# Optimization experiments

Hardware: AMD Instinct MI355X
Metric: run time of the kernel (lower is better)

## Reference

```python
import jax, jax.numpy as jnp
import numpy as np

N = 50000          # masked node count
E = 800000         # edges (avg degree 16)
IN_DIM, GCN_DIM, REL_DIM, TRAIN_DIM, OUT_DIM = 3, 128, 64, 128, 2
BATCHES = 1


def setup_inputs() -> dict:
    key = jax.random.key(0)
    ks = jax.random.split(key, 16)
    s = 0.05
    return {
        "features": jax.random.normal(ks[0], (N, IN_DIM), jnp.float32),
        "edge_index": jax.random.randint(ks[1], (2, E), 0, N, dtype=jnp.int32),
        "trainOT": jax.random.normal(ks[2], (TRAIN_DIM,), jnp.float32),
        "W1": jax.random.normal(ks[3], (IN_DIM, GCN_DIM), jnp.float32) * s,
        "b1": jnp.zeros((GCN_DIM,), jnp.float32),
        "W2": jax.random.normal(ks[4], (GCN_DIM, GCN_DIM), jnp.float32) * s,
        "b2": jnp.zeros((GCN_DIM,), jnp.float32),
        "Wq": jax.random.normal(ks[5], (GCN_DIM, REL_DIM), jnp.float32) * s,
        "bq": jnp.zeros((REL_DIM,), jnp.float32),
        "Wk": jax.random.normal(ks[6], (TRAIN_DIM, REL_DIM), jnp.float32) * s,
        "bk": jnp.zeros((REL_DIM,), jnp.float32),
        "Wv": jax.random.normal(ks[7], (GCN_DIM, TRAIN_DIM), jnp.float32) * s,
        "bv": jnp.zeros((TRAIN_DIM,), jnp.float32),
        "Ws": jax.random.normal(ks[8], (TRAIN_DIM, OUT_DIM * N), jnp.float32) * s,
        "bs": jnp.zeros((OUT_DIM * N,), jnp.float32),
    }


def _gcn_conv(x, W, b, src, dst, n):
    """PyG GCNConv: h = D^-1/2 (A+I) D^-1/2 (x W) + b (self-loops already in src/dst)."""
    h = x @ W                                                  # [n, d_out]
    ones = jnp.ones(src.shape[0], dtype=x.dtype)
    deg = jax.ops.segment_sum(ones, dst, num_segments=n)      # in-degree incl. self-loop
    dinv = jnp.where(deg > 0, jax.lax.rsqrt(deg), 0.0)
    norm = dinv[src] * dinv[dst]                               # [E+n]
    msg = h[src] * norm[:, None]                               # gather (dominant traffic)
    return jax.ops.segment_sum(msg, dst, num_segments=n) + b   # scatter-add


def reference(features, edge_index, trainOT, W1, b1, W2, b2, Wq, bq, Wk, bk, Wv, bv, Ws, bs):
    n = features.shape[0]
    loop = jnp.arange(n, dtype=edge_index.dtype)
    src = jnp.concatenate([edge_index[0], loop])
    dst = jnp.concatenate([edge_index[1], loop])

    h1 = jax.nn.relu(_gcn_conv(features, W1, b1, src, dst, n))   # gcn1 + relu
    h2 = _gcn_conv(h1, W2, b2, src, dst, n)                      # gcn2

    q = h2 @ Wq + bq                                             # [n, rel]
    v = h2 @ Wv + bv                                             # [n, train]
    k = trainOT @ Wk + bk                                        # [rel]
    scale = jnp.asarray(Wq.shape[1], q.dtype) ** 0.5
    rel = jax.nn.sigmoid((q @ k) / scale)                        # [n]
    summed_idea = (rel[:, None] * v).sum(axis=0)                 # [train]
    new_trainOT = trainOT + summed_idea
    speak = new_trainOT @ Ws + bs                                # [out_dim * num_nodes]
    out = speak.reshape(BATCHES, -1, OUT_DIM)
    return out, new_trainOT
```

## Files before the change

### kernel.cpp

```cpp
#include <hip/hip_runtime.h>
#include <math.h>

#define O_ROWPTR (256*1024)
#define O_DINV   (512*1024)
#define O_SMALL  (768*1024)
#define O_GHIST  (1024*1024)
#define O_BSTART (1256*1024)
#define O_GOFF   (1280*1024)
#define O_SORT   (1536*1024)
#define O_PART   (1536*1024)
#define O_XS     (4800*1024)
#define O_COL    (5760*1024)
#define O_H1     (9216*1024)

#define LAYER2_BLOCKS 2048
#define NCHUNK 256

static __device__ __forceinline__ unsigned int f2bf(float f) {
    unsigned int u = __float_as_uint(f);
    return (u + 0x7fffu + ((u >> 16) & 1u)) >> 16;
}
static __device__ __forceinline__ float bf_lo(unsigned int w) { return __uint_as_float(w << 16); }
static __device__ __forceinline__ float bf_hi(unsigned int w) { return __uint_as_float(w & 0xffff0000u); }

static __device__ __forceinline__ int blockExclScan256(int v, volatile int* lds, int t) {
    int lane = t & 63, wid = t >> 6;
    int incl = v;
#pragma unroll
    for (int off = 1; off < 64; off <<= 1) {
        int n = __shfl_up(incl, off);
        if (lane >= off) incl += n;
    }
    if (lane == 63) lds[wid] = incl;
    __syncthreads();
    if (t == 0) {
        int s = 0;
#pragma unroll
        for (int i = 0; i < 4; ++i) { int x = lds[i]; lds[i] = s; s += x; }
    }
    __syncthreads();
    return lds[wid] + incl - v;
}

__global__ void k_hist(const int* __restrict__ dst, int* __restrict__ ghist,
                       int E, int CS, int NB) {
    __shared__ int lh[256];
    int b = blockIdx.x, t = threadIdx.x;
    lh[t] = 0; __syncthreads();
    int s = b * CS, e = min(E, s + CS);
    for (int i = s + t; i < e; i += 256) {
        atomicAdd(&lh[dst[i] >> 8], 1);
    }
    __syncthreads();
    if (t < NB) ghist[t * NCHUNK + b] = lh[t];
}

__global__ void k_bstart(const int* __restrict__ ghist, int* __restrict__ bstart, int NB) {
    __shared__ int lds[4];
    int t = threadIdx.x;
    int v = 0;
    if (t < NB) {
        const int* row = ghist + t * NCHUNK;
        for (int b = 0; b < NCHUNK; ++b) v += row[b];
    }
    int ex = blockExclScan256(v, lds, t);
    if (t <= NB) bstart[t] = ex;
}

__global__ void k_goff(const int* __restrict__ ghist, const int* __restrict__ bstart,
                       int* __restrict__ goff, int NB) {
    __shared__ int lds1[4];
    int nb = blockIdx.x, t = threadIdx.x;
    int base = bstart[nb];
    int g = ghist[nb * NCHUNK + t];
    int gx = blockExclScan256(g, lds1, t);
    goff[nb * NCHUNK + t] = base + gx;
}

__global__ void k_scatter(const int* __restrict__ src, const int* __restrict__ dst,
                          const int* __restrict__ goff, unsigned int* __restrict__ sorted,
                          int E, int CS, int NB) {
    __shared__ int lcur[256];
    int b = blockIdx.x, t = threadIdx.x;
    if (t < NB) lcur[t] = goff[t * NCHUNK + b];
    __syncthreads();
    int s = b * CS, e = min(E, s + CS);
    for (int i = s + t; i < e; i += 256) {
        int d = dst[i];
        int pos = atomicAdd(&lcur[d >> 8], 1);
        sorted[pos] = ((unsigned int)(d & 255) << 16) | (unsigned int)src[i];
    }
}

__global__ void k_build(const unsigned int* __restrict__ sorted, const int* __restrict__ bstart,
                        int* __restrict__ row_ptr, int* __restrict__ col,
                        float* __restrict__ dinv, int N, int NB) {
    __shared__ int lcnt[256];
    __shared__ int lpos[256];
    __shared__ int lds1[4];
    int nb = blockIdx.x, t = threadIdx.x;
    lcnt[t] = 0; __syncthreads();
    int s = bstart[nb], e = bstart[nb + 1];
    for (int i = s + t; i < e; i += 256) {
        atomicAdd(&lcnt[sorted[i] >> 16], 1);
    }
    __syncthreads();
    int c = lcnt[t];
    int cx = blockExclScan256(c, lds1, t);
    int rp = s + cx;
    int node = (nb << 8) + t;
    row_ptr[node] = rp;
    lpos[t] = rp;
    if (node < N) dinv[node] = rsqrtf((float)(c + 1));
    __syncthreads();
    for (int i = s + t; i < e; i += 256) {
        unsigned int v = sorted[i];
        int p = atomicAdd(&lpos[v >> 16], 1);
        col[p] = (int)(v & 0xffffu);
    }
}

__global__ void k_prep(const float* __restrict__ dinv, const float* __restrict__ x,
                       const float* __restrict__ bs, float* __restrict__ out,
                       float4* __restrict__ xs4, unsigned int* __restrict__ h1s, int N) {
    int i = blockIdx.x * blockDim.x + threadIdx.x;
    if (i < N) {
        float d = dinv[i];
        float4 v;
        v.x = x[i * 3] * d; v.y = x[i * 3 + 1] * d; v.z = x[i * 3 + 2] * d; v.w = 0.f;
        xs4[i] = v;
        reinterpret_cast<float2*>(out)[i] = reinterpret_cast<const float2*>(bs)[i];
    }
    if (i < 64) h1s[(size_t)N * 64 + i] = 0u;
}

__global__ void k_tiny1(const float* __restrict__ trainOT, const float* __restrict__ Wq,
                        const float* __restrict__ bq, const float* __restrict__ Wk,
                        const float* __restrict__ bk, const float* __restrict__ W2,
                        const float* __restrict__ b2, float* __restrict__ small) {
    __shared__ float kv[64];
    __shared__ float wqk[128];
    __shared__ float red[128];
    int t = threadIdx.x;
    if (t < 64) {
        float acc = bk[t];
        for (int j = 0; j < 128; ++j) acc += trainOT[j] * Wk[j * 64 + t];
        kv[t] = acc;
    }
    __syncthreads();
    float accq = 0.f;
    for (int c = 0; c < 64; ++c) accq += Wq[t * 64 + c] * kv[c];
    wqk[t] = accq;
    red[t] = (t < 64) ? bq[t] * kv[t] : 0.f;
    __syncthreads();
    for (int off = 64; off >= 1; off >>= 1) { if (t < off) red[t] += red[t + off]; __syncthreads(); }
    float bqs = red[0];
    __syncthreads();
    float acc2 = 0.f;
    for (int j = 0; j < 128; ++j) acc2 += W2[t * 128 + j] * wqk[j];
    small[t] = acc2;
    red[t] = b2[t] * wqk[t];
    __syncthreads();
    for (int off = 64; off >= 1; off >>= 1) { if (t < off) red[t] += red[t + off]; __syncthreads(); }
    if (t == 0) small[128] = bqs + red[0];
}

__global__ void k_layer1(const float4* __restrict__ xs4, const int* __restrict__ row_ptr,
                         const int* __restrict__ col, const float* __restrict__ dinv,
                         const float* __restrict__ W1, const float* __restrict__ b1,
                         unsigned int* __restrict__ h1s, int N) {
    int t = threadIdx.x;
    int sub = t & 15;
    int node = blockIdx.x * 16 + (t >> 4);
    if (node >= N) return;
    float di = dinv[node];
    int s = row_ptr[node], e = row_ptr[node + 1];
    float a0 = 0.f, a1 = 0.f, a2 = 0.f;
    for (int j = s + sub; j < e; j += 16) {
        float4 xv = xs4[col[j]];
        a0 += xv.x; a1 += xv.y; a2 += xv.z;
    }
    if (sub == 0) { float4 xv = xs4[node]; a0 += xv.x; a1 += xv.y; a2 += xv.z; }
#pragma unroll
    for (int off = 1; off < 16; off <<= 1) {
        a0 += __shfl_xor(a0, off);
        a1 += __shfl_xor(a1, off);
        a2 += __shfl_xor(a2, off);
    }
    a0 *= di; a1 *= di; a2 *= di;
    unsigned int p[4];
#pragma unroll
    for (int m = 0; m < 4; ++m) {
        int c = 8 * sub + 2 * m;
        float vlo = fmaxf(a0 * W1[c]     + a1 * W1[128 + c]     + a2 * W1[256 + c]     + b1[c],     0.f) * di;
        float vhi = fmaxf(a0 * W1[c + 1] + a1 * W1[128 + c + 1] + a2 * W1[256 + c + 1] + b1[c + 1], 0.f) * di;
        p[m] = f2bf(vlo) | (f2bf(vhi) << 16);
    }
    uint4 st; st.x = p[0]; st.y = p[1]; st.z = p[2]; st.w = p[3];
    reinterpret_cast<uint4*>(h1s + (size_t)node * 64)[sub] = st;
}

__global__ void k_layer2(const unsigned int* __restrict__ h1s, const int* __restrict__ row_ptr,
                         const int* __restrict__ col, const float* __restrict__ dinv,
                         const float* __restrict__ small, float* __restrict__ part, int N) {
    int t = threadIdx.x, lane = t & 63, wid = t >> 6;
    int sub = lane & 15, grp = lane >> 4;
    int wg = blockIdx.x * 4 + wid;
    const int nwaves = LAYER2_BLOCKS * 4;
    float w2[8];
#pragma unroll
    for (int j = 0; j < 8; ++j) w2[j] = small[8 * sub + j];
    float bias = small[128];
    float sacc[8];
#pragma unroll
    for (int j = 0; j < 8; ++j) sacc[j] = 0.f;
    float sR = 0.f;

    for (int node = wg; node < N; node += nwaves) {
        float di = dinv[node];
        int s = row_ptr[node], e = row_ptr[node + 1];
        int items = e - s + 1;
        float acc[8];
#pragma unroll
        for (int j = 0; j < 8; ++j) acc[j] = 0.f;
        for (int base = 0; base < items; base += 8) {
            int q0 = base + grp, q1 = base + 4 + grp;
            int u0 = (q0 == 0) ? node : ((q0 < items) ? col[s + q0 - 1] : N);
            int u1 = (q1 < items) ? col[s + q1 - 1] : N;
            uint4 v0 = reinterpret_cast<const uint4*>(h1s + (size_t)u0 * 64)[sub];
            uint4 v1 = reinterpret_cast<const uint4*>(h1s + (size_t)u1 * 64)[sub];
            acc[0] += bf_lo(v0.x) + bf_lo(v1.x);
            acc[1] += bf_hi(v0.x) + bf_hi(v1.x);
            acc[2] += bf_lo(v0.y) + bf_lo(v1.y);
            acc[3] += bf_hi(v0.y) + bf_hi(v1.y);
            acc[4] += bf_lo(v0.z) + bf_lo(v1.z);
            acc[5] += bf_hi(v0.z) + bf_hi(v1.z);
            acc[6] += bf_lo(v0.w) + bf_lo(v1.w);
            acc[7] += bf_hi(v0.w) + bf_hi(v1.w);
        }
#pragma unroll
        for (int j = 0; j < 8; ++j) {
            acc[j] += __shfl_xor(acc[j], 16);
            acc[j] += __shfl_xor(acc[j], 32);
        }
        float dv = 0.f;
#pragma unroll
        for (int j = 0; j < 8; ++j) dv += acc[j] * w2[j];
#pragma unroll
        for (int off = 1; off < 16; off <<= 1) dv += __shfl_xor(dv, off);
        float z = (dv * di + bias) * 0.125f;
        float rel = 1.f / (1.f + __expf(-z));
        float rd = rel * di;
#pragma unroll
        for (int j = 0; j < 8; ++j) sacc[j] += rd * acc[j];
        sR += rel;
    }
    __shared__ float sS[4][132];
    if (grp == 0) {
#pragma unroll
        for (int j = 0; j < 8; ++j) sS[wid][8 * sub + j] = sacc[j];
    }
    if (lane == 0) sS[wid][128] = sR;
    __syncthreads();
    if (t < 129) part[blockIdx.x * 132 + t] = sS[0][t] + sS[1][t] + sS[2][t] + sS[3][t];
}

__global__ void k_reduce_part(const float* __restrict__ part, int nblocks, float* __restrict__ small) {
    int c = blockIdx.x;
    float acc = 0.f;
    for (int b = threadIdx.x; b < nblocks; b += blockDim.x) acc += part[b * 132 + c];
    __shared__ float sd[256];
    sd[threadIdx.x] = acc; __syncthreads();
    for (int off = 128; off; off >>= 1) { if (threadIdx.x < off) sd[threadIdx.x] += sd[threadIdx.x + off]; __syncthreads(); }
    if (threadIdx.x == 0) small[132 + c] = sd[0];
}

__global__ void k_tiny2(const float* __restrict__ trainOT, const float* __restrict__ W2,
                        const float* __restrict__ b2, const float* __restrict__ Wv,
                        const float* __restrict__ bv, float* __restrict__ small,
                        float* __restrict__ out_tail) {
    __shared__ float t1[128];
    int t = threadIdx.x;
    float R = small[260];
    float acc = R * b2[t];
    for (int j = 0; j < 128; ++j) acc += small[132 + j] * W2[j * 128 + t];
    t1[t] = acc; __syncthreads();
    float acc2 = R * bv[t];
    for (int j = 0; j < 128; ++j) acc2 += t1[j] * Wv[j * 128 + t];
    float nt = trainOT[t] + acc2;
    small[264 + t] = nt;
    out_tail[t] = nt;
}

__global__ void k_tail(const float* __restrict__ Ws, const float* __restrict__ small,
                       float* __restrict__ out, int out_n) {
    int ks = blockIdx.x & 3;
    int j = ((blockIdx.x >> 2) << 8) + threadIdx.x;
    if (j >= out_n) return;
    const float* w = Ws + (size_t)(ks * 32) * out_n + j;
    const float* nt = small + 264 + ks * 32;
    float acc = 0.f;
#pragma unroll 8
    for (int k = 0; k < 32; ++k) acc += nt[k] * w[(size_t)k * out_n];
    atomicAdd(&out[j], acc);
}

extern "C" void kernel_launch(void* const* d_in, const int* in_sizes, int n_in,
                              void* d_out, int out_size, void* d_ws, size_t ws_size,
                              hipStream_t stream) {
    const float* features = (const float*)d_in[0];
    const int*   eidx     = (const int*)d_in[1];
    const float* trainOT  = (const float*)d_in[2];
    const float* W1 = (const float*)d_in[3];
    const float* b1 = (const float*)d_in[4];
    const float* W2 = (const float*)d_in[5];
    const float* b2 = (const float*)d_in[6];
    const float* Wq = (const float*)d_in[7];
    const float* bq = (const float*)d_in[8];
    const float* Wk = (const float*)d_in[9];
    const float* bk = (const float*)d_in[10];
    const float* Wv = (const float*)d_in[11];
    const float* bv = (const float*)d_in[12];
    const float* Ws = (const float*)d_in[13];
    const float* bs = (const float*)d_in[14];

    int N = in_sizes[0] / 3;
    int E = in_sizes[1] / 2;
    const int* esrc = eidx;
    const int* edst = eidx + E;
    int NB = (N + 255) >> 8;
    int CS = (E + NCHUNK - 1) / NCHUNK;

    char* ws = (char*)d_ws;
    int*   row_ptr = (int*)(ws + O_ROWPTR);
    float* dinv    = (float*)(ws + O_DINV);
    float* small   = (float*)(ws + O_SMALL);
    int*   ghist   = (int*)(ws + O_GHIST);
    int*   bstart  = (int*)(ws + O_BSTART);
    int*   goff    = (int*)(ws + O_GOFF);
    unsigned int* sorted = (unsigned int*)(ws + O_SORT);
    float* part    = (float*)(ws + O_PART);
    float4* xs4    = (float4*)(ws + O_XS);
    int*   col     = (int*)(ws + O_COL);
    unsigned int* h1s = (unsigned int*)(ws + O_H1);
    float* out     = (float*)d_out;
    int out_n = out_size - 128;

    k_tiny1<<<1, 128, 0, stream>>>(trainOT, Wq, bq, Wk, bk, W2, b2, small);
    k_hist<<<NCHUNK, 256, 0, stream>>>(edst, ghist, E, CS, NB);
    k_bstart<<<1, 256, 0, stream>>>(ghist, bstart, NB);
    k_goff<<<NB, 256, 0, stream>>>(ghist, bstart, goff, NB);
    k_scatter<<<NCHUNK, 256, 0, stream>>>(esrc, edst, goff, sorted, E, CS, NB);
    k_build<<<NB, 256, 0, stream>>>(sorted, bstart, row_ptr, col, dinv, N, NB);
    k_prep<<<(N + 255) / 256, 256, 0, stream>>>(dinv, features, bs, out, xs4, h1s, N);
    k_layer1<<<(N + 15) / 16, 256, 0, stream>>>(xs4, row_ptr, col, dinv, W1, b1, h1s, N);
    k_layer2<<<LAYER2_BLOCKS, 256, 0, stream>>>(h1s, row_ptr, col, dinv, small, part, N);
    k_reduce_part<<<129, 256, 0, stream>>>(part, LAYER2_BLOCKS, small);
    k_tiny2<<<1, 128, 0, stream>>>(trainOT, W2, b2, Wv, bv, small, out + out_n);
    k_tail<<<((out_n + 255) / 256) * 4, 256, 0, stream>>>(Ws, small, out, out_n);
}
```

Baseline: 115.6 us.

## Reassociate layer-2 aggregation into scalar gathers using a reverse CSR

Layer 2 used to gather 128-wide bf16 rows for every edge. Now layer 1 projects each h1 row onto a precomputed vector to get one scalar y per node. A scalar gather of y gives rel. The attention-weighted sum is then computed by gathering the scalar rel*dinv over a source-sorted (transposed) CSR, and each node's h1 row is read only once. This swaps the per-edge 256-byte gathers for 4-byte gathers, at the cost of building a second CSR (doubling the sort and histogram work) and adding a kernel launch; k_prep is also folded into k_build.

```diff
diff --git a/kernel.cpp b/kernel.cpp
--- a/kernel.cpp
+++ b/kernel.cpp
@@ -1,20 +1,29 @@
 #include <hip/hip_runtime.h>
 #include <math.h>
 
-#define O_ROWPTR (256*1024)
+#define O_RPD    (0)
+#define O_RPS    (256*1024)
 #define O_DINV   (512*1024)
 #define O_SMALL  (768*1024)
-#define O_GHIST  (1024*1024)
-#define O_BSTART (1256*1024)
-#define O_GOFF   (1280*1024)
-#define O_SORT   (1536*1024)
-#define O_PART   (1536*1024)
-#define O_XS     (4800*1024)
-#define O_COL    (5760*1024)
-#define O_H1     (9216*1024)
-
-#define LAYER2_BLOCKS 2048
+#define O_Y      (1024*1024)
+#define O_RELW   (1280*1024)
+#define O_REL    (1536*1024)
+#define O_GHD    (1792*1024)
+#define O_GHS    (2048*1024)
+#define O_GOD    (2304*1024)
+#define O_GOS    (2560*1024)
+#define O_BSD    (2816*1024)
+#define O_BSS    (2944*1024)
+#define O_PART   (3072*1024)
+#define O_XS     (3712*1024)
+#define O_SRTD   (4608*1024)
+#define O_SRTS   (11776*1024 - 3584*1024)
+#define O_COLD   (11776*1024)
+#define O_COLS   (15360*1024)
+#define O_H1     (18688*1024)
+
 #define NCHUNK 256
+#define ZBLOCKS 1024
 
 static __device__ __forceinline__ unsigned int f2bf(float f) {
     unsigned int u = __float_as_uint(f);
@@ -42,96 +51,110 @@
     return lds[wid] + incl - v;
 }
 
-__global__ void k_hist(const int* __restrict__ dst, int* __restrict__ ghist,
-                       int E, int CS, int NB) {
+__global__ void k_hist(const int* __restrict__ eidx, int* __restrict__ ghD,
+                       int* __restrict__ ghS, int E, int CS, int NB) {
     __shared__ int lh[256];
     int b = blockIdx.x, t = threadIdx.x;
+    const int* arr = blockIdx.y ? eidx : (eidx + E);
+    int* gh = blockIdx.y ? ghS : ghD;
     lh[t] = 0; __syncthreads();
     int s = b * CS, e = min(E, s + CS);
-    for (int i = s + t; i < e; i += 256) {
-        atomicAdd(&lh[dst[i] >> 8], 1);
-    }
-    __syncthreads();
-    if (t < NB) ghist[t * NCHUNK + b] = lh[t];
-}
-
-__global__ void k_bstart(const int* __restrict__ ghist, int* __restrict__ bstart, int NB) {
-    __shared__ int lds[4];
-    int t = threadIdx.x;
-    int v = 0;
+    for (int i = s + t; i < e; i += 256) atomicAdd(&lh[arr[i] >> 8], 1);
+    __syncthreads();
+    if (t < NB) gh[t * NCHUNK + b] = lh[t];
+}
+
+__global__ void k_bstart(const int* __restrict__ ghD, const int* __restrict__ ghS,
+                         int* __restrict__ bsD, int* __restrict__ bsS, int NB) {
+    __shared__ int lds1[4];
+    __shared__ int lds2[4];
+    int t = threadIdx.x;
+    int vD = 0, vS = 0;
     if (t < NB) {
-        const int* row = ghist + t * NCHUNK;
-        for (int b = 0; b < NCHUNK; ++b) v += row[b];
-    }
-    int ex = blockExclScan256(v, lds, t);
-    if (t <= NB) bstart[t] = ex;
-}
-
-__global__ void k_goff(const int* __restrict__ ghist, const int* __restrict__ bstart,
-                       int* __restrict__ goff, int NB) {
+        const int* rD = ghD + t * NCHUNK;
+        const int* rS = ghS + t * NCHUNK;
+        for (int b = 0; b < NCHUNK; ++b) { vD += rD[b]; vS += rS[b]; }
+    }
+    int exD = blockExclScan256(vD, lds1, t);
+    if (t <= NB) bsD[t] = exD;
+    __syncthreads();
+    int exS = blockExclScan256(vS, lds2, t);
+    if (t <= NB) bsS[t] = exS;
+}
+
+__global__ void k_goff(const int* __restrict__ ghD, const int* __restrict__ ghS,
+                       const int* __restrict__ bsD, const int* __restrict__ bsS,
+                       int* __restrict__ goD, int* __restrict__ goS, int NB) {
     __shared__ int lds1[4];
     int nb = blockIdx.x, t = threadIdx.x;
-    int base = bstart[nb];
-    int g = ghist[nb * NCHUNK + t];
+    const int* gh = blockIdx.y ? ghS : ghD;
+    const int* bs = blockIdx.y ? bsS : bsD;
+    int* go = blockIdx.y ? goS : goD;
+    int base = bs[nb];
+    int g = gh[nb * NCHUNK + t];
     int gx = blockExclScan256(g, lds1, t);
-    goff[nb * NCHUNK + t] = base + gx;
-}
-
-__global__ void k_scatter(const int* __restrict__ src, const int* __restrict__ dst,
-                          const int* __restrict__ goff, unsigned int* __restrict__ sorted,
-                          int E, int CS, int NB) {
+    go[nb * NCHUNK + t] = base + gx;
+}
+
+__global__ void k_scatter(const int* __restrict__ eidx, const int* __restrict__ goD,
+                          const int* __restrict__ goS, unsigned int* __restrict__ srtD,
+                          unsigned int* __restrict__ srtS, int E, int CS, int NB) {
     __shared__ int lcur[256];
     int b = blockIdx.x, t = threadIdx.x;
-    if (t < NB) lcur[t] = goff[t * NCHUNK + b];
+    const int* key = blockIdx.y ? eidx : (eidx + E);
+    const int* val = blockIdx.y ? (eidx + E) : eidx;
+    const int* go  = blockIdx.y ? goS : goD;
+    unsigned int* srt = blockIdx.y ? srtS : srtD;
+    if (t < NB) lcur[t] = go[t * NCHUNK + b];
     __syncthreads();
     int s = b * CS, e = min(E, s + CS);
     for (int i = s + t; i < e; i += 256) {
-        int d = dst[i];
-        int pos = atomicAdd(&lcur[d >> 8], 1);
-        sorted[pos] = ((unsigned int)(d & 255) << 16) | (unsigned int)src[i];
-    }
-}
-
-__global__ void k_build(const unsigned int* __restrict__ sorted, const int* __restrict__ bstart,
-                        int* __restrict__ row_ptr, int* __restrict__ col,
-                        float* __restrict__ dinv, int N, int NB) {
+        int k = key[i];
+        int pos = atomicAdd(&lcur[k >> 8], 1);
+        srt[pos] = ((unsigned int)(k & 255) << 16) | (unsigned int)val[i];
+    }
+}
+
+__global__ void k_build(const unsigned int* __restrict__ srtD, const unsigned int* __restrict__ srtS,
+                        const int* __restrict__ bsD, const int* __restrict__ bsS,
+                        int* __restrict__ rpD, int* __restrict__ rpS,
+                        int* __restrict__ colD, int* __restrict__ colS,
+                        float* __restrict__ dinv, const float* __restrict__ x,
+                        float4* __restrict__ xs4, const float* __restrict__ bs,
+                        float* __restrict__ out, int N, int NB) {
     __shared__ int lcnt[256];
     __shared__ int lpos[256];
     __shared__ int lds1[4];
     int nb = blockIdx.x, t = threadIdx.x;
+    bool rev = blockIdx.y != 0;
+    const unsigned int* srt = rev ? srtS : srtD;
+    const int* bst = rev ? bsS : bsD;
+    int* rp  = rev ? rpS : rpD;
+    int* col = rev ? colS : colD;
     lcnt[t] = 0; __syncthreads();
-    int s = bstart[nb], e = bstart[nb + 1];
-    for (int i = s + t; i < e; i += 256) {
-        atomicAdd(&lcnt[sorted[i] >> 16], 1);
-    }
+    int s = bst[nb], e = bst[nb + 1];
+    for (int i = s + t; i < e; i += 256) atomicAdd(&lcnt[srt[i] >> 16], 1);
     __syncthreads();
     int c = lcnt[t];
     int cx = blockExclScan256(c, lds1, t);
-    int rp = s + cx;
+    int rpv = s + cx;
     int node = (nb << 8) + t;
-    row_ptr[node] = rp;
-    lpos[t] = rp;
-    if (node < N) dinv[node] = rsqrtf((float)(c + 1));
+    rp[node] = rpv;
+    lpos[t] = rpv;
+    if (!rev && node < N) {
+        float d = rsqrtf((float)(c + 1));
+        dinv[node] = d;
+        float4 v;
+        v.x = x[node * 3] * d; v.y = x[node * 3 + 1] * d; v.z = x[node * 3 + 2] * d; v.w = 0.f;
+        xs4[node] = v;
+        reinterpret_cast<float2*>(out)[node] = reinterpret_cast<const float2*>(bs)[node];
+    }
     __syncthreads();
     for (int i = s + t; i < e; i += 256) {
-        unsigned int v = sorted[i];
+        unsigned int v = srt[i];
         int p = atomicAdd(&lpos[v >> 16], 1);
         col[p] = (int)(v & 0xffffu);
     }
-}
-
-__global__ void k_prep(const float* __restrict__ dinv, const float* __restrict__ x,
-                       const float* __restrict__ bs, float* __restrict__ out,
-                       float4* __restrict__ xs4, unsigned int* __restrict__ h1s, int N) {
-    int i = blockIdx.x * blockDim.x + threadIdx.x;
-    if (i < N) {
-        float d = dinv[i];
-        float4 v;
-        v.x = x[i * 3] * d; v.y = x[i * 3 + 1] * d; v.z = x[i * 3 + 2] * d; v.w = 0.f;
-        xs4[i] = v;
-        reinterpret_cast<float2*>(out)[i] = reinterpret_cast<const float2*>(bs)[i];
-    }
-    if (i < 64) h1s[(size_t)N * 64 + i] = 0u;
 }
 
 __global__ void k_tiny1(const float* __restrict__ trainOT, const float* __restrict__ Wq,
@@ -165,19 +188,20 @@
     if (t == 0) small[128] = bqs + red[0];
 }
 
-__global__ void k_layer1(const float4* __restrict__ xs4, const int* __restrict__ row_ptr,
-                         const int* __restrict__ col, const float* __restrict__ dinv,
+__global__ void k_layer1(const float4* __restrict__ xs4, const int* __restrict__ rpD,
+                         const int* __restrict__ colD, const float* __restrict__ dinv,
                          const float* __restrict__ W1, const float* __restrict__ b1,
-                         unsigned int* __restrict__ h1s, int N) {
+                         const float* __restrict__ small, unsigned int* __restrict__ h1s,
+                         float* __restrict__ y, int N) {
     int t = threadIdx.x;
     int sub = t & 15;
     int node = blockIdx.x * 16 + (t >> 4);
     if (node >= N) return;
     float di = dinv[node];
-    int s = row_ptr[node], e = row_ptr[node + 1];
+    int s = rpD[node], e = rpD[node + 1];
     float a0 = 0.f, a1 = 0.f, a2 = 0.f;
     for (int j = s + sub; j < e; j += 16) {
-        float4 xv = xs4[col[j]];
+        float4 xv = xs4[colD[j]];
         a0 += xv.x; a1 += xv.y; a2 += xv.z;
     }
     if (sub == 0) { float4 xv = xs4[node]; a0 += xv.x; a1 += xv.y; a2 += xv.z; }
@@ -189,78 +213,76 @@
     }
     a0 *= di; a1 *= di; a2 *= di;
     unsigned int p[4];
+    float yl = 0.f;
 #pragma unroll
     for (int m = 0; m < 4; ++m) {
         int c = 8 * sub + 2 * m;
         float vlo = fmaxf(a0 * W1[c]     + a1 * W1[128 + c]     + a2 * W1[256 + c]     + b1[c],     0.f) * di;
         float vhi = fmaxf(a0 * W1[c + 1] + a1 * W1[128 + c + 1] + a2 * W1[256 + c + 1] + b1[c + 1], 0.f) * di;
         p[m] = f2bf(vlo) | (f2bf(vhi) << 16);
+        yl += bf_lo(p[m]) * small[c] + bf_hi(p[m]) * small[c + 1];
     }
     uint4 st; st.x = p[0]; st.y = p[1]; st.z = p[2]; st.w = p[3];
     reinterpret_cast<uint4*>(h1s + (size_t)node * 64)[sub] = st;
-}
-
-__global__ void k_layer2(const unsigned int* __restrict__ h1s, const int* __restrict__ row_ptr,
-                         const int* __restrict__ col, const float* __restrict__ dinv,
-                         const float* __restrict__ small, float* __restrict__ part, int N) {
+#pragma unroll
+    for (int off = 1; off < 16; off <<= 1) yl += __shfl_xor(yl, off);
+    if (sub == 0) y[node] = yl;
+}
+
+__global__ void k_dv(const float* __restrict__ y, const int* __restrict__ rpD,
+                     const int* __restrict__ colD, const float* __restrict__ dinv,
+                     const float* __restrict__ small, float* __restrict__ relw,
+                     float* __restrict__ rel, int N) {
+    int t = threadIdx.x;
+    int sub = t & 15;
+    int node = blockIdx.x * 16 + (t >> 4);
+    if (node >= N) return;
+    float di = dinv[node];
+    int s = rpD[node], e = rpD[node + 1];
+    float acc = (sub == 0) ? y[node] : 0.f;
+    for (int j = s + sub; j < e; j += 16) acc += y[colD[j]];
+#pragma unroll
+    for (int off = 1; off < 16; off <<= 1) acc += __shfl_xor(acc, off);
+    float z = (acc * di + small[128]) * 0.125f;
+    float r = 1.f / (1.f + __expf(-z));
+    if (sub == 0) { rel[node] = r; relw[node] = r * di; }
+}
+
+__global__ void k_z(const unsigned int* __restrict__ h1s, const int* __restrict__ rpS,
+                    const int* __restrict__ colS, const float* __restrict__ relw,
+                    const float* __restrict__ rel, float* __restrict__ part, int N) {
     int t = threadIdx.x, lane = t & 63, wid = t >> 6;
-    int sub = lane & 15, grp = lane >> 4;
-    int wg = blockIdx.x * 4 + wid;
-    const int nwaves = LAYER2_BLOCKS * 4;
-    float w2[8];
-#pragma unroll
-    for (int j = 0; j < 8; ++j) w2[j] = small[8 * sub + j];
-    float bias = small[128];
-    float sacc[8];
-#pragma unroll
-    for (int j = 0; j < 8; ++j) sacc[j] = 0.f;
-    float sR = 0.f;
-
-    for (int node = wg; node < N; node += nwaves) {
-        float di = dinv[node];
-        int s = row_ptr[node], e = row_ptr[node + 1];
-        int items = e - s + 1;
-        float acc[8];
-#pragma unroll
-        for (int j = 0; j < 8; ++j) acc[j] = 0.f;
-        for (int base = 0; base < items; base += 8) {
-            int q0 = base + grp, q1 = base + 4 + grp;
-            int u0 = (q0 == 0) ? node : ((q0 < items) ? col[s + q0 - 1] : N);
-            int u1 = (q1 < items) ? col[s + q1 - 1] : N;
-            uint4 v0 = reinterpret_cast<const uint4*>(h1s + (size_t)u0 * 64)[sub];
-            uint4 v1 = reinterpret_cast<const uint4*>(h1s + (size_t)u1 * 64)[sub];
-            acc[0] += bf_lo(v0.x) + bf_lo(v1.x);
-            acc[1] += bf_hi(v0.x) + bf_hi(v1.x);
-            acc[2] += bf_lo(v0.y) + bf_lo(v1.y);
-            acc[3] += bf_hi(v0.y) + bf_hi(v1.y);
-            acc[4] += bf_lo(v0.z) + bf_lo(v1.z);
-            acc[5] += bf_hi(v0.z) + bf_hi(v1.z);
-            acc[6] += bf_lo(v0.w) + bf_lo(v1.w);
-            acc[7] += bf_hi(v0.w) + bf_hi(v1.w);
-        }
-#pragma unroll
-        for (int j = 0; j < 8; ++j) {
-            acc[j] += __shfl_xor(acc[j], 16);
-            acc[j] += __shfl_xor(acc[j], 32);
-        }
-        float dv = 0.f;
-#pragma unroll
-        for (int j = 0; j < 8; ++j) dv += acc[j] * w2[j];
-#pragma unroll
-        for (int off = 1; off < 16; off <<= 1) dv += __shfl_xor(dv, off);
-        float z = (dv * di + bias) * 0.125f;
-        float rel = 1.f / (1.f + __expf(-z));
-        float rd = rel * di;
-#pragma unroll
-        for (int j = 0; j < 8; ++j) sacc[j] += rd * acc[j];
-        sR += rel;
-    }
+    int sub = lane & 15;
+    float acc[8];
+#pragma unroll
+    for (int j = 0; j < 8; ++j) acc[j] = 0.f;
+    float Racc = 0.f;
+    for (int node = blockIdx.x * 16 + (t >> 4); node < N; node += ZBLOCKS * 16) {
+        int s = rpS[node], e = rpS[node + 1];
+        float w = (sub == 0) ? relw[node] : 0.f;
+        for (int j = s + sub; j < e; j += 16) w += relw[colS[j]];
+#pragma unroll
+        for (int off = 1; off < 16; off <<= 1) w += __shfl_xor(w, off);
+        uint4 v = reinterpret_cast<const uint4*>(h1s + (size_t)node * 64)[sub];
+        acc[0] += w * bf_lo(v.x); acc[1] += w * bf_hi(v.x);
+        acc[2] += w * bf_lo(v.y); acc[3] += w * bf_hi(v.y);
+        acc[4] += w * bf_lo(v.z); acc[5] += w * bf_hi(v.z);
+        acc[6] += w * bf_lo(v.w); acc[7] += w * bf_hi(v.w);
+        if (sub == 0) Racc += rel[node];
+    }
+#pragma unroll
+    for (int j = 0; j < 8; ++j) {
+        acc[j] += __shfl_xor(acc[j], 16);
+        acc[j] += __shfl_xor(acc[j], 32);
+    }
+    Racc += __shfl_xor(Racc, 16);
+    Racc += __shfl_xor(Racc, 32);
     __shared__ float sS[4][132];
-    if (grp == 0) {
-#pragma unroll
-        for (int j = 0; j < 8; ++j) sS[wid][8 * sub + j] = sacc[j];
-    }
-    if (lane == 0) sS[wid][128] = sR;
+    if (lane < 16) {
+#pragma unroll
+        for (int j = 0; j < 8; ++j) sS[wid][8 * sub + j] = acc[j];
+    }
+    if (lane == 0) sS[wid][128] = Racc;
     __syncthreads();
     if (t < 129) part[blockIdx.x * 132 + t] = sS[0][t] + sS[1][t] + sS[2][t] + sS[3][t];
 }
@@ -326,36 +348,44 @@
 
     int N = in_sizes[0] / 3;
     int E = in_sizes[1] / 2;
-    const int* esrc = eidx;
-    const int* edst = eidx + E;
     int NB = (N + 255) >> 8;
     int CS = (E + NCHUNK - 1) / NCHUNK;
 
     char* ws = (char*)d_ws;
-    int*   row_ptr = (int*)(ws + O_ROWPTR);
-    float* dinv    = (float*)(ws + O_DINV);
-    float* small   = (float*)(ws + O_SMALL);
-    int*   ghist   = (int*)(ws + O_GHIST);
-    int*   bstart  = (int*)(ws + O_BSTART);
-    int*   goff    = (int*)(ws + O_GOFF);
-    unsigned int* sorted = (unsigned int*)(ws + O_SORT);
-    float* part    = (float*)(ws + O_PART);
-    float4* xs4    = (float4*)(ws + O_XS);
-    int*   col     = (int*)(ws + O_COL);
+    int*   rpD   = (int*)(ws + O_RPD);
+    int*   rpS   = (int*)(ws + O_RPS);
+    float* dinv  = (float*)(ws + O_DINV);
+    float* small = (float*)(ws + O_SMALL);
+    float* y     = (float*)(ws + O_Y);
+    float* relw  = (float*)(ws + O_RELW);
+    float* rel   = (float*)(ws + O_REL);
+    int*   ghD   = (int*)(ws + O_GHD);
+    int*   ghS   = (int*)(ws + O_GHS);
+    int*   goD   = (int*)(ws + O_GOD);
+    int*   goS   = (int*)(ws + O_GOS);
+    int*   bsD   = (int*)(ws + O_BSD);
+    int*   bsS   = (int*)(ws + O_BSS);
+    float* part  = (float*)(ws + O_PART);
+    float4* xs4  = (float4*)(ws + O_XS);
+    unsigned int* srtD = (unsigned int*)(ws + O_SRTD);
+    unsigned int* srtS = (unsigned int*)(ws + O_SRTS);
+    int*   colD  = (int*)(ws + O_COLD);
+    int*   colS  = (int*)(ws + O_COLS);
     unsigned int* h1s = (unsigned int*)(ws + O_H1);
-    float* out     = (float*)d_out;
+    float* out   = (float*)d_out;
     int out_n = out_size - 128;
 
     k_tiny1<<<1, 128, 0, stream>>>(trainOT, Wq, bq, Wk, bk, W2, b2, small);
-    k_hist<<<NCHUNK, 256, 0, stream>>>(edst, ghist, E, CS, NB);
-    k_bstart<<<1, 256, 0, stream>>>(ghist, bstart, NB);
-    k_goff<<<NB, 256, 0, stream>>>(ghist, bstart, goff, NB);
-    k_scatter<<<NCHUNK, 256, 0, stream>>>(esrc, edst, goff, sorted, E, CS, NB);
-    k_build<<<NB, 256, 0, stream>>>(sorted, bstart, row_ptr, col, dinv, N, NB);
-    k_prep<<<(N + 255) / 256, 256, 0, stream>>>(dinv, features, bs, out, xs4, h1s, N);
-    k_layer1<<<(N + 15) / 16, 256, 0, stream>>>(xs4, row_ptr, col, dinv, W1, b1, h1s, N);
-    k_layer2<<<LAYER2_BLOCKS, 256, 0, stream>>>(h1s, row_ptr, col, dinv, small, part, N);
-    k_reduce_part<<<129, 256, 0, stream>>>(part, LAYER2_BLOCKS, small);
+    k_hist<<<dim3(NCHUNK, 2), 256, 0, stream>>>(eidx, ghD, ghS, E, CS, NB);
+    k_bstart<<<1, 256, 0, stream>>>(ghD, ghS, bsD, bsS, NB);
+    k_goff<<<dim3(NB, 2), 256, 0, stream>>>(ghD, ghS, bsD, bsS, goD, goS, NB);
+    k_scatter<<<dim3(NCHUNK, 2), 256, 0, stream>>>(eidx, goD, goS, srtD, srtS, E, CS, NB);
+    k_build<<<dim3(NB, 2), 256, 0, stream>>>(srtD, srtS, bsD, bsS, rpD, rpS, colD, colS,
+                                             dinv, features, xs4, bs, out, N, NB);
+    k_layer1<<<(N + 15) / 16, 256, 0, stream>>>(xs4, rpD, colD, dinv, W1, b1, small, h1s, y, N);
+    k_dv<<<(N + 15) / 16, 256, 0, stream>>>(y, rpD, colD, dinv, small, relw, rel, N);
+    k_z<<<ZBLOCKS, 256, 0, stream>>>(h1s, rpS, colS, relw, rel, part, N);
+    k_reduce_part<<<129, 256, 0, stream>>>(part, ZBLOCKS, small);
     k_tiny2<<<1, 128, 0, stream>>>(trainOT, W2, b2, Wv, bv, small, out + out_n);
     k_tail<<<((out_n + 255) / 256) * 4, 256, 0, stream>>>(Ws, small, out, out_n);
 }
```

Result: faster. 113.0 us (-2.3%).
